# Kernel optimization log

Hardware: AMD Instinct MI355X
Metric: run time of the kernel (lower is better)

The kernel has to match this reference:

```python
import jax, jax.numpy as jnp
import numpy as np

B, N, E = 4, 10000, 160000
FIN, H, FO = 256, 8, 32
NEG_SLOPE = 0.2
MASK_FILL = -9e15  # matches torch's 9e15*(mask-1) sentinel


def setup_inputs() -> dict:
    key = jax.random.key(0)
    ks = jax.random.split(key, 7)
    x = jax.random.normal(ks[0], (B, N, FIN), dtype=jnp.float32)
    edge_index = jax.random.randint(ks[1], (B, 2, E), 0, N, dtype=jnp.int64)
    edge_mask = jnp.ones((B, E), dtype=jnp.float32)
    W = jax.random.normal(ks[2], (H * FO, FIN), dtype=jnp.float32) * (1.0 / np.sqrt(FIN))
    a_src = jax.random.normal(ks[3], (H, FO), dtype=jnp.float32) * 0.1
    a_trg = jax.random.normal(ks[4], (H, FO), dtype=jnp.float32) * 0.1
    bias = jax.random.normal(ks[5], (H * FO,), dtype=jnp.float32) * 0.01
    return {"x": x, "edge_index": edge_index, "edge_mask": edge_mask,
            "W": W, "a_src": a_src, "a_trg": a_trg, "bias": bias}


def reference(x, edge_index, edge_mask, W, a_src, a_trg, bias):
    # Dropout is identity in eval mode (reference baseline).
    b, n, fin = x.shape
    h, fo = a_src.shape
    # linear projection: [B,N,Fin] @ W^T -> [B,N,H,Fo]
    proj = (x @ W.T).reshape(b, n, h, fo)
    # per-node source/target scores: [B*N, H]
    s_src = jnp.einsum('bnhf,hf->bnh', proj, a_src).reshape(b * n, h)
    s_trg = jnp.einsum('bnhf,hf->bnh', proj, a_trg).reshape(b * n, h)
    projf = proj.reshape(b * n, h, fo)
    # offset node ids per batch and flatten edges: [2, B*E]
    ei = edge_index + (jnp.arange(b, dtype=edge_index.dtype) * n)[:, None, None]
    ei = jnp.transpose(ei, (1, 0, 2)).reshape(2, -1)
    src, trg = ei[0], ei[1]
    mask = edge_mask.reshape(-1)  # [B*E]
    # lift + LeakyReLU edge scores: [B*E, H]
    scores = jax.nn.leaky_relu(s_src[src] + s_trg[trg], negative_slope=NEG_SLOPE)
    scores = jnp.where(mask[:, None] > 0, scores, jnp.float32(MASK_FILL))
    # neighborhood (segment) softmax over target node
    ex = jnp.exp(scores)
    den = jax.ops.segment_sum(ex, trg, num_segments=b * n)  # [B*N, H]
    attn = ex / (den[trg] + 1e-16)                           # [B*E, H]
    # weighted scatter-add aggregation
    weighted = projf[src] * attn[:, :, None]                 # [B*E, H, Fo]
    out = jax.ops.segment_sum(weighted, trg, num_segments=b * n)
    # concat heads, add bias, ELU activation
    out = out.reshape(b, n, h * fo) + bias
    return jax.nn.elu(out)
```

## Files before the change

### kernel.cpp

```cpp
#include <hip/hip_runtime.h>
#include <hip/hip_bf16.h>

#define BB   4
#define NN   10000
#define EE   160000
#define FIN  256
#define HH   8
#define FO   32
#define CC   256
#define BN   40000
#define BE   640000
#define CAP  48
#define DStr 16

#define XCVT 5000
#define WCVT 32
#define DZB  625
#define WBB  8
#define GMB  626
#define CLB  625
#define SCB  1250

typedef __attribute__((ext_vector_type(8))) __bf16 bf16x8;
typedef __attribute__((ext_vector_type(4))) float  f32x4;

__device__ __forceinline__ float bf2f(unsigned short u) {
    unsigned int v = ((unsigned int)u) << 16;
    return __uint_as_float(v);
}
__device__ __forceinline__ unsigned short f2bf(float f) {
    unsigned int u = __float_as_uint(f);
    u += 0x7fffu + ((u >> 16) & 1u);
    return (unsigned short)(u >> 16);
}

__device__ __forceinline__ void cvt8(const float* __restrict__ src,
                                     unsigned short* __restrict__ dst, int i)
{
    const float4* s = (const float4*)src + (size_t)i * 2;
    float4 v0 = s[0], v1 = s[1];
    float f[8] = {v0.x, v0.y, v0.z, v0.w, v1.x, v1.y, v1.z, v1.w};
    union { unsigned short u[8]; uint4 q; } o;
#pragma unroll
    for (int j = 0; j < 8; ++j) o.u[j] = f2bf(f[j]);
    ((uint4*)dst)[i] = o.q;
}

__global__ __launch_bounds__(256) void k_prep(
    const float* __restrict__ x, const float* __restrict__ Wm,
    const float* __restrict__ a_src, const float* __restrict__ a_trg,
    unsigned short* __restrict__ xb, unsigned short* __restrict__ wb,
    int* __restrict__ deg, float* __restrict__ wsrcg,
    float* __restrict__ wtrgg)
{
    int blk = blockIdx.x, t = threadIdx.x;
    if (blk < XCVT) {
        cvt8(x, xb, blk * 256 + t);
    } else if (blk < XCVT + WCVT) {
        cvt8(Wm, wb, (blk - XCVT) * 256 + t);
    } else if (blk < XCVT + WCVT + DZB) {
        int i = (blk - XCVT - WCVT) * 256 + t;
        if (i < BN * DStr / 4) ((uint4*)deg)[i] = make_uint4(0, 0, 0, 0);
    } else {
        int h = blk - XCVT - WCVT - DZB;
        int k = t;
        float s = 0.f, tg = 0.f;
#pragma unroll
        for (int f = 0; f < FO; ++f) {
            float w = Wm[(size_t)(h * FO + f) * FIN + k];
            s  += a_src[h * FO + f] * w;
            tg += a_trg[h * FO + f] * w;
        }
        wsrcg[h * FIN + k] = s;
        wtrgg[h * FIN + k] = tg;
    }
}

__global__ __launch_bounds__(256) void k_main(
    const unsigned short* __restrict__ xb, const unsigned short* __restrict__ wb,
    unsigned short* __restrict__ proj, const int* __restrict__ ei,
    const float* __restrict__ mask, int* __restrict__ deg,
    int* __restrict__ esrc, const float* __restrict__ wsrcg,
    const float* __restrict__ wtrgg, float* __restrict__ ssrc,
    float* __restrict__ strg)
{
    __shared__ alignas(16) unsigned char smem[32768];
    const int t = threadIdx.x;
    const int blk = blockIdx.x;
    const int role = blk & 3;
    const int rid  = blk >> 2;

    if (role >= 2) {
        int sid = rid * 2 + (role - 2);
        float* ws = (float*)smem;
        float* wt = ws + 8 * 257;
        for (int i = t; i < 8 * FIN; i += 256) {
            int hh = i >> 8, kk = i & 255;
            ws[hh * 257 + kk] = wsrcg[i];
            wt[hh * 257 + kk] = wtrgg[i];
        }
        __syncthreads();
        int node = sid * 32 + (t >> 3);
        int h    = t & 7;
        const uint4* xr = (const uint4*)(xb + (size_t)node * FIN);
        const float* pw = ws + h * 257;
        const float* pt = wt + h * 257;
        float vs = 0.f, vt = 0.f;
#pragma unroll
        for (int i = 0; i < 32; ++i) {
            uint4 q = xr[i];
            unsigned int v[4] = {q.x, q.y, q.z, q.w};
#pragma unroll
            for (int j = 0; j < 4; ++j) {
                float lo = __uint_as_float(v[j] << 16);
                float hi = __uint_as_float(v[j] & 0xffff0000u);
                int c = i * 8 + j * 2;
                vs += lo * pw[c] + hi * pw[c + 1];
                vt += lo * pt[c] + hi * pt[c + 1];
            }
        }
        ssrc[(size_t)node * HH + h] = vs;
        strg[(size_t)node * HH + h] = vt;
        return;
    }

    if (role == 1) {
        int i = rid * 256 + t;
        int e0 = i * 4;
        int b  = e0 / EE;
        int le = e0 - b * EE;
        const int* eb = ei + (size_t)b * 2 * EE;
        int4   sq = *(const int4*)(eb + le);
        int4   tq = *(const int4*)(eb + EE + le);
        float4 mq = *(const float4*)(mask + e0);
        int base = b * NN;

        int t0 = tq.x + base, t1 = tq.y + base, t2 = tq.z + base, t3 = tq.w + base;
        int p0 = atomicAdd(&deg[t0 * DStr], 1);
        int p1 = atomicAdd(&deg[t1 * DStr], 1);
        int p2 = atomicAdd(&deg[t2 * DStr], 1);
        int p3 = atomicAdd(&deg[t3 * DStr], 1);
        if (p0 < CAP) esrc[t0 * CAP + p0] = (sq.x + base) | (mq.x > 0.f ? 0 : (int)0x80000000);
        if (p1 < CAP) esrc[t1 * CAP + p1] = (sq.y + base) | (mq.y > 0.f ? 0 : (int)0x80000000);
        if (p2 < CAP) esrc[t2 * CAP + p2] = (sq.z + base) | (mq.z > 0.f ? 0 : (int)0x80000000);
        if (p3 < CAP) esrc[t3 * CAP + p3] = (sq.w + base) | (mq.w > 0.f ? 0 : (int)0x80000000);
        return;
    }

    unsigned short* As = (unsigned short*)smem;
    unsigned short* Bs = (unsigned short*)(smem + 16384);
    const int lane = t & 63;
    const int wid  = t >> 6;
    const int wr   = wid >> 1, wc = wid & 1;
    const int bm   = rid >> 1;
    const int bn   = rid & 1;
    const int row0 = bm * 128, col0 = bn * 128;

    const int srow = t >> 3;
    const int scol = (t & 7) * 8;

    f32x4 acc[4][4] = {};

    for (int kt = 0; kt < 4; ++kt) {
        const int k0 = kt * 64;
#pragma unroll
        for (int p = 0; p < 4; ++p) {
            int tr = p * 32 + srow;
            int cg = scol ^ ((tr & 7) << 3);
            int gra = row0 + tr; if (gra > BN - 1) gra = BN - 1;
            const unsigned short* ga = xb + (size_t)gra * FIN + k0 + cg;
            const unsigned short* gb = wb + (size_t)(col0 + tr) * FIN + k0 + cg;
            __builtin_amdgcn_global_load_lds(
                (const __attribute__((address_space(1))) void*)ga,
                (__attribute__((address_space(3))) void*)&As[p * 2048 + t * 8],
                16, 0, 0);
            __builtin_amdgcn_global_load_lds(
                (const __attribute__((address_space(1))) void*)gb,
                (__attribute__((address_space(3))) void*)&Bs[p * 2048 + t * 8],
                16, 0, 0);
        }
        __syncthreads();

#pragma unroll
        for (int kk = 0; kk < 2; ++kk) {
            bf16x8 af[4], bfr[4];
#pragma unroll
            for (int m = 0; m < 4; ++m) {
                int row = wr * 64 + m * 16 + (lane & 15);
                int col = (kk * 32 + (lane >> 4) * 8) ^ ((row & 7) << 3);
                af[m] = *(const bf16x8*)&As[row * 64 + col];
            }
#pragma unroll
            for (int n = 0; n < 4; ++n) {
                int row = wc * 64 + n * 16 + (lane & 15);
                int col = (kk * 32 + (lane >> 4) * 8) ^ ((row & 7) << 3);
                bfr[n] = *(const bf16x8*)&Bs[row * 64 + col];
            }
#pragma unroll
            for (int m = 0; m < 4; ++m)
#pragma unroll
                for (int n = 0; n < 4; ++n)
                    acc[m][n] = __builtin_amdgcn_mfma_f32_16x16x32_bf16(
                        af[m], bfr[n], acc[m][n], 0, 0, 0);
        }
        __syncthreads();
    }

    const int rbase = row0 + wr * 64 + (lane >> 4) * 4;
    const int cbase = col0 + wc * 64 + (lane & 15);
#pragma unroll
    for (int m = 0; m < 4; ++m)
#pragma unroll
        for (int n = 0; n < 4; ++n)
#pragma unroll
            for (int j = 0; j < 4; ++j) {
                int r = rbase + m * 16 + j;
                int c = cbase + n * 16;
                if (r < BN) proj[(size_t)r * CC + c] = f2bf(acc[m][n][j]);
            }
}

__global__ __launch_bounds__(256) void k_gather(
    const int* __restrict__ deg, const int* __restrict__ esrc,
    const float* __restrict__ ssrc, const float* __restrict__ strg,
    const unsigned short* __restrict__ proj, const float* __restrict__ bias,
    float* __restrict__ out)
{
    int gid  = blockIdx.x * 256 + threadIdx.x;
    int node = gid >> 6;
    int lane = gid & 63;
    if (node >= BN) return;
    int h  = lane >> 3;
    int el = lane & 7;
    int hb = lane & 56;
    float st = strg[(size_t)node * HH + h];
    int cnt = deg[node * DStr]; if (cnt > CAP) cnt = CAP;
    const int lo = node * CAP;

    int sv = (lane < cnt) ? esrc[lo + lane] : (int)0x80000000;

    const char* projc = (const char*)proj;
    const unsigned lb = lane * 8u;

    float acc0 = 0.f, acc1 = 0.f, acc2 = 0.f, acc3 = 0.f, deno = 0.f;

    int  svo = __shfl(sv, el);
    float f  = ssrc[(size_t)(svo & 0x7fffffff) * HH + h];

    const int ng = (cnt + 7) >> 3;
    for (int g = 0; g < ng; ++g) {
        int  svn = __shfl(sv, ((g + 1) * 8 + el) & 63);
        float fn = ssrc[(size_t)(svn & 0x7fffffff) * HH + h];

        float c = f + st;
        c = c > 0.f ? c : 0.2f * c;
        float ex = (svo >= 0) ? __expf(c) : 0.f;
        deno += ex;

#pragma unroll
        for (int e = 0; e < 8; ++e) {
            float ee = __shfl(ex, e | hb);
            int   se = __shfl(sv, g * 8 + e) & 0x7fffffff;
            ushort4 q = *(const ushort4*)(projc + (((unsigned)se << 9) + lb));
            acc0 += bf2f(q.x) * ee;
            acc1 += bf2f(q.y) * ee;
            acc2 += bf2f(q.z) * ee;
            acc3 += bf2f(q.w) * ee;
        }
        svo = svn; f = fn;
    }

#pragma unroll
    for (int off = 1; off < 8; off <<= 1) deno += __shfl_xor(deno, off);

    float inv = 1.f / (deno + 1e-16f);
    float4 bv = ((const float4*)bias)[lane];
    float o0 = acc0 * inv + bv.x, o1 = acc1 * inv + bv.y;
    float o2 = acc2 * inv + bv.z, o3 = acc3 * inv + bv.w;
    o0 = o0 > 0.f ? o0 : __expf(o0) - 1.f;
    o1 = o1 > 0.f ? o1 : __expf(o1) - 1.f;
    o2 = o2 > 0.f ? o2 : __expf(o2) - 1.f;
    o3 = o3 > 0.f ? o3 : __expf(o3) - 1.f;
    ((float4*)(out + (size_t)node * CC))[lane] = make_float4(o0, o1, o2, o3);
}

extern "C" void kernel_launch(void* const* d_in, const int* in_sizes, int n_in,
                              void* d_out, int out_size, void* d_ws, size_t ws_size,
                              hipStream_t stream)
{
    const float* x     = (const float*)d_in[0];
    const int*   ei    = (const int*)  d_in[1];
    const float* mask  = (const float*)d_in[2];
    const float* Wm    = (const float*)d_in[3];
    const float* a_src = (const float*)d_in[4];
    const float* a_trg = (const float*)d_in[5];
    const float* bias  = (const float*)d_in[6];
    float* out = (float*)d_out;

    char* ws = (char*)d_ws;
    size_t off = 0;
    unsigned short* xb = (unsigned short*)(ws + off); off += (size_t)BN * FIN * 2;
    unsigned short* wb = (unsigned short*)(ws + off); off += (size_t)CC * FIN * 2;
    unsigned short* proj = (unsigned short*)(ws + off); off += (size_t)BN * CC * 2;
    float* ssrc  = (float*)(ws + off); off += (size_t)BN * HH * 4;
    float* strg  = (float*)(ws + off); off += (size_t)BN * HH * 4;
    float* wsrcg = (float*)(ws + off); off += (size_t)HH * FIN * 4;
    float* wtrgg = (float*)(ws + off); off += (size_t)HH * FIN * 4;
    int*   deg   = (int*)  (ws + off); off += (size_t)BN * DStr * 4;
    int*   esrc  = (int*)  (ws + off); off += (size_t)BN * CAP * 4;

    k_prep  <<<XCVT + WCVT + DZB + WBB, 256, 0, stream>>>(
        x, Wm, a_src, a_trg, xb, wb, deg, wsrcg, wtrgg);
    k_main  <<<GMB + CLB + SCB, 256, 0, stream>>>(
        xb, wb, proj, ei, mask, deg, esrc, wsrcg, wtrgg, ssrc, strg);
    k_gather<<<(BN * 64) / 256, 256, 0, stream>>>(
        deg, esrc, ssrc, strg, proj, bias, out);
}
```

Baseline: 92.62 us.

## Move edge claiming into prep kernel and zero degrees with memset

The edge-bucketing role (atomic degree claims and esrc writes) moves out of the main GEMM/score kernel into the prep kernel, where it runs alongside the bf16 conversion blocks. The degree array is now cleared by a hipMemsetAsync before the prep kernel, replacing the zeroing blocks that used to run inside it. The main kernel now interleaves only the GEMM and score roles, split three ways by blk%3. This shortens the critical kernel and overlaps the atomic-heavy work with bandwidth-bound conversion, at the cost of an extra memset launch.

New measurement: 109.9 us. 18.6% more time.

```diff
diff --git a/kernel.cpp b/kernel.cpp
--- a/kernel.cpp
+++ b/kernel.cpp
@@ -13,12 +13,11 @@
 #define CAP  48
 #define DStr 16
 
+#define CLB  625
 #define XCVT 5000
 #define WCVT 32
-#define DZB  625
 #define WBB  8
 #define GMB  626
-#define CLB  625
 #define SCB  1250
 
 typedef __attribute__((ext_vector_type(8))) __bf16 bf16x8;
@@ -46,86 +45,17 @@
     ((uint4*)dst)[i] = o.q;
 }
 
-__global__ __launch_bounds__(256) void k_prep(
+__global__ __launch_bounds__(256) void k_prepclaim(
     const float* __restrict__ x, const float* __restrict__ Wm,
     const float* __restrict__ a_src, const float* __restrict__ a_trg,
+    const int* __restrict__ ei, const float* __restrict__ mask,
     unsigned short* __restrict__ xb, unsigned short* __restrict__ wb,
-    int* __restrict__ deg, float* __restrict__ wsrcg,
-    float* __restrict__ wtrgg)
+    int* __restrict__ deg, int* __restrict__ esrc,
+    float* __restrict__ wsrcg, float* __restrict__ wtrgg)
 {
     int blk = blockIdx.x, t = threadIdx.x;
-    if (blk < XCVT) {
-        cvt8(x, xb, blk * 256 + t);
-    } else if (blk < XCVT + WCVT) {
-        cvt8(Wm, wb, (blk - XCVT) * 256 + t);
-    } else if (blk < XCVT + WCVT + DZB) {
-        int i = (blk - XCVT - WCVT) * 256 + t;
-        if (i < BN * DStr / 4) ((uint4*)deg)[i] = make_uint4(0, 0, 0, 0);
-    } else {
-        int h = blk - XCVT - WCVT - DZB;
-        int k = t;
-        float s = 0.f, tg = 0.f;
-#pragma unroll
-        for (int f = 0; f < FO; ++f) {
-            float w = Wm[(size_t)(h * FO + f) * FIN + k];
-            s  += a_src[h * FO + f] * w;
-            tg += a_trg[h * FO + f] * w;
-        }
-        wsrcg[h * FIN + k] = s;
-        wtrgg[h * FIN + k] = tg;
-    }
-}
-
-__global__ __launch_bounds__(256) void k_main(
-    const unsigned short* __restrict__ xb, const unsigned short* __restrict__ wb,
-    unsigned short* __restrict__ proj, const int* __restrict__ ei,
-    const float* __restrict__ mask, int* __restrict__ deg,
-    int* __restrict__ esrc, const float* __restrict__ wsrcg,
-    const float* __restrict__ wtrgg, float* __restrict__ ssrc,
-    float* __restrict__ strg)
-{
-    __shared__ alignas(16) unsigned char smem[32768];
-    const int t = threadIdx.x;
-    const int blk = blockIdx.x;
-    const int role = blk & 3;
-    const int rid  = blk >> 2;
-
-    if (role >= 2) {
-        int sid = rid * 2 + (role - 2);
-        float* ws = (float*)smem;
-        float* wt = ws + 8 * 257;
-        for (int i = t; i < 8 * FIN; i += 256) {
-            int hh = i >> 8, kk = i & 255;
-            ws[hh * 257 + kk] = wsrcg[i];
-            wt[hh * 257 + kk] = wtrgg[i];
-        }
-        __syncthreads();
-        int node = sid * 32 + (t >> 3);
-        int h    = t & 7;
-        const uint4* xr = (const uint4*)(xb + (size_t)node * FIN);
-        const float* pw = ws + h * 257;
-        const float* pt = wt + h * 257;
-        float vs = 0.f, vt = 0.f;
-#pragma unroll
-        for (int i = 0; i < 32; ++i) {
-            uint4 q = xr[i];
-            unsigned int v[4] = {q.x, q.y, q.z, q.w};
-#pragma unroll
-            for (int j = 0; j < 4; ++j) {
-                float lo = __uint_as_float(v[j] << 16);
-                float hi = __uint_as_float(v[j] & 0xffff0000u);
-                int c = i * 8 + j * 2;
-                vs += lo * pw[c] + hi * pw[c + 1];
-                vt += lo * pt[c] + hi * pt[c + 1];
-            }
-        }
-        ssrc[(size_t)node * HH + h] = vs;
-        strg[(size_t)node * HH + h] = vt;
-        return;
-    }
-
-    if (role == 1) {
-        int i = rid * 256 + t;
+    if (blk < CLB) {
+        int i = blk * 256 + t;
         int e0 = i * 4;
         int b  = e0 / EE;
         int le = e0 - b * EE;
@@ -144,6 +74,69 @@
         if (p1 < CAP) esrc[t1 * CAP + p1] = (sq.y + base) | (mq.y > 0.f ? 0 : (int)0x80000000);
         if (p2 < CAP) esrc[t2 * CAP + p2] = (sq.z + base) | (mq.z > 0.f ? 0 : (int)0x80000000);
         if (p3 < CAP) esrc[t3 * CAP + p3] = (sq.w + base) | (mq.w > 0.f ? 0 : (int)0x80000000);
+    } else if (blk < CLB + XCVT) {
+        cvt8(x, xb, (blk - CLB) * 256 + t);
+    } else if (blk < CLB + XCVT + WCVT) {
+        cvt8(Wm, wb, (blk - CLB - XCVT) * 256 + t);
+    } else {
+        int h = blk - CLB - XCVT - WCVT;
+        int k = t;
+        float s = 0.f, tg = 0.f;
+#pragma unroll
+        for (int f = 0; f < FO; ++f) {
+            float w = Wm[(size_t)(h * FO + f) * FIN + k];
+            s  += a_src[h * FO + f] * w;
+            tg += a_trg[h * FO + f] * w;
+        }
+        wsrcg[h * FIN + k] = s;
+        wtrgg[h * FIN + k] = tg;
+    }
+}
+
+__global__ __launch_bounds__(256) void k_main(
+    const unsigned short* __restrict__ xb, const unsigned short* __restrict__ wb,
+    unsigned short* __restrict__ proj, const float* __restrict__ wsrcg,
+    const float* __restrict__ wtrgg, float* __restrict__ ssrc,
+    float* __restrict__ strg)
+{
+    __shared__ alignas(16) unsigned char smem[32768];
+    const int t = threadIdx.x;
+    const int blk = blockIdx.x;
+    const int role = blk % 3;
+    const int rid  = blk / 3;
+
+    if (role >= 1) {
+        int sid = rid * 2 + (role - 1);
+        if (sid >= SCB) return;
+        float* ws = (float*)smem;
+        float* wt = ws + 8 * 257;
+        for (int i = t; i < 8 * FIN; i += 256) {
+            int hh = i >> 8, kk = i & 255;
+            ws[hh * 257 + kk] = wsrcg[i];
+            wt[hh * 257 + kk] = wtrgg[i];
+        }
+        __syncthreads();
+        int node = sid * 32 + (t >> 3);
+        int h    = t & 7;
+        const uint4* xr = (const uint4*)(xb + (size_t)node * FIN);
+        const float* pw = ws + h * 257;
+        const float* pt = wt + h * 257;
+        float vs = 0.f, vt = 0.f;
+#pragma unroll
+        for (int i = 0; i < 32; ++i) {
+            uint4 q = xr[i];
+            unsigned int v[4] = {q.x, q.y, q.z, q.w};
+#pragma unroll
+            for (int j = 0; j < 4; ++j) {
+                float lo = __uint_as_float(v[j] << 16);
+                float hi = __uint_as_float(v[j] & 0xffff0000u);
+                int c = i * 8 + j * 2;
+                vs += lo * pw[c] + hi * pw[c + 1];
+                vt += lo * pt[c] + hi * pt[c + 1];
+            }
+        }
+        ssrc[(size_t)node * HH + h] = vs;
+        strg[(size_t)node * HH + h] = vt;
         return;
     }
 
@@ -309,10 +302,11 @@
     int*   deg   = (int*)  (ws + off); off += (size_t)BN * DStr * 4;
     int*   esrc  = (int*)  (ws + off); off += (size_t)BN * CAP * 4;
 
-    k_prep  <<<XCVT + WCVT + DZB + WBB, 256, 0, stream>>>(
-        x, Wm, a_src, a_trg, xb, wb, deg, wsrcg, wtrgg);
-    k_main  <<<GMB + CLB + SCB, 256, 0, stream>>>(
-        xb, wb, proj, ei, mask, deg, esrc, wsrcg, wtrgg, ssrc, strg);
+    hipMemsetAsync(deg, 0, (size_t)BN * DStr * 4, stream);
+    k_prepclaim<<<CLB + XCVT + WCVT + WBB, 256, 0, stream>>>(
+        x, Wm, a_src, a_trg, ei, mask, xb, wb, deg, esrc, wsrcg, wtrgg);
+    k_main  <<<3 * GMB, 256, 0, stream>>>(
+        xb, wb, proj, wsrcg, wtrgg, ssrc, strg);
     k_gather<<<(BN * 64) / 256, 256, 0, stream>>>(
         deg, esrc, ssrc, strg, proj, bias, out);
 }
```
